# Performance work log

Hardware: AMD Instinct MI355X
Metric: run time of the kernel (lower is better)

## Reference

```python
import jax, jax.numpy as jnp
import numpy as np

B, S, D = 2, 1024, 1024
L, E, F = 2, 8, 2048


def setup_inputs() -> dict:
    key = jax.random.key(0)
    kx, kp, k1, k2 = jax.random.split(key, 4)
    x = jax.random.normal(kx, (B, S, D), dtype=jnp.float32)
    # prototypes scaled so dot products are O(1), keeping softmax well-behaved
    protos = jax.random.normal(kp, (L, E, D), dtype=jnp.float32) / np.sqrt(D)
    W1 = jax.random.normal(k1, (L, E, D, F), dtype=jnp.float32) * 0.02
    W2 = jax.random.normal(k2, (L, E, F, D), dtype=jnp.float32) * 0.02
    return {"x": x, "protos": protos, "W1": W1, "W2": W2, "k": 2}


def _route(x, protos_l, k):
    # expert_mapping: abs(dot(prototype, input)) per expert, keep top-k, rest -> -inf, softmax
    scores = jnp.abs(jnp.einsum("bsd,ed->bse", x, protos_l))  # [B,S,E]
    topv, _ = jax.lax.top_k(scores, k)
    thresh = topv[..., -1:]  # k-th largest per token
    masked = jnp.where(scores >= thresh, scores, -jnp.inf)
    return jax.nn.softmax(masked, axis=-1)  # [B,S,E]


def reference(x, protos, W1, W2, k):
    n_layers = protos.shape[0]
    for l in range(n_layers):  # fixed small layer loop
        w = _route(x, protos[l], k)  # [B,S,E]
        h = jax.nn.relu(jnp.einsum("bsd,edf->bsef", x, W1[l]))  # [B,S,E,F]
        y = jnp.einsum("bsef,efd,bse->bsd", h, W2[l], w)  # weighted expert mix
        x = x + y
    return x
```

## Files before the change

### kernel.cpp

```cpp
#include <hip/hip_runtime.h>
#include <hip/hip_bf16.h>
#include <cstdint>

#define T_TOKENS 2048
#define DDIM 1024
#define FDIM 2048
#define NEXP 8
#define NLAYER 2
#define BMPAD 64
#define RMAX 4608
#define RALLOC 4736

#define ATILE_EL 2048
#define BTILE_EL 4096

typedef unsigned short u16;
typedef short bf16x8 __attribute__((ext_vector_type(8)));
typedef u16 u16x8 __attribute__((ext_vector_type(8)));
typedef u16 u16x4v __attribute__((ext_vector_type(4)));
typedef float f32x4 __attribute__((ext_vector_type(4)));

#define VMCNT(n) asm volatile("s_waitcnt vmcnt(" #n ")" ::: "memory")
#define SB() __builtin_amdgcn_sched_barrier(0)
#define BAR() __builtin_amdgcn_s_barrier()

__device__ __forceinline__ u16 bf16_rn(float f) {
  unsigned u = __builtin_bit_cast(unsigned, f);
  u += 0x7fffu + ((u >> 16) & 1u);
  return (u16)(u >> 16);
}
__device__ __forceinline__ float bf16_f(u16 h) {
  unsigned u = ((unsigned)h) << 16;
  return __builtin_bit_cast(float, u);
}

__device__ __forceinline__ void gl16(const void* g, void* l) {
  __builtin_amdgcn_global_load_lds((const __attribute__((address_space(1))) void*)g,
                                   (__attribute__((address_space(3))) void*)l, 16, 0, 0);
}

__device__ __forceinline__ void xcd_swizzle(int& bx, int& by, int& bz) {
  const unsigned gx = gridDim.x, gy = gridDim.y;
  const unsigned lin = blockIdx.x + gx * (blockIdx.y + gy * blockIdx.z);
  const unsigned nwg = gx * gy * gridDim.z;
  const unsigned nl = (lin & 7u) * (nwg >> 3) + (lin >> 3);
  bx = nl % gx;
  const unsigned t = nl / gx;
  by = t % gy;
  bz = t / gy;
}

__global__ __launch_bounds__(256) void route_kernel(
    const float* __restrict__ x, const float* __restrict__ protos,
    int* __restrict__ eid, float* __restrict__ wgt) {
  const int t = blockIdx.x;
  const int tid = threadIdx.x;
  const float4* xr4 = (const float4*)(x + (size_t)t * DDIM);
  const float4* pr4 = (const float4*)protos;
  __shared__ float red[NEXP][256];
  const float4 xv = xr4[tid];
  float acc[NEXP];
#pragma unroll
  for (int e = 0; e < NEXP; ++e) {
    const float4 p = pr4[e * 256 + tid];
    acc[e] = xv.x * p.x + xv.y * p.y + xv.z * p.z + xv.w * p.w;
  }
#pragma unroll
  for (int e = 0; e < NEXP; ++e) red[e][tid] = acc[e];
  __syncthreads();
  for (int s = 128; s > 0; s >>= 1) {
    if (tid < s) {
#pragma unroll
      for (int e = 0; e < NEXP; ++e) red[e][tid] += red[e][tid + s];
    }
    __syncthreads();
  }
  if (tid == 0) {
    float m1 = -1.f, m2 = -1.f;
    int i1 = 0, i2 = 0;
#pragma unroll
    for (int e = 0; e < NEXP; ++e) {
      float s = fabsf(red[e][0]);
      if (s > m1) { m2 = m1; i2 = i1; m1 = s; i1 = e; }
      else if (s > m2) { m2 = s; i2 = e; }
    }
    float e2 = __expf(m2 - m1);
    float z = 1.f + e2;
    eid[t * 2] = i1;
    eid[t * 2 + 1] = i2;
    wgt[t * 2] = 1.f / z;
    wgt[t * 2 + 1] = e2 / z;
  }
}

__global__ __launch_bounds__(256) void route2_kernel(
    const float* __restrict__ x, const float* __restrict__ protos2,
    const u16* __restrict__ h_hi, const u16* __restrict__ h_lo,
    const float* __restrict__ P, const int* __restrict__ eidA,
    const int* __restrict__ pos, const float* __restrict__ wgtA,
    int* __restrict__ eidB, float* __restrict__ wgtB) {
  const int t = blockIdx.x;
  const int tid = threadIdx.x;
  __shared__ float red[NEXP][256];
  const float4 xv = ((const float4*)(x + (size_t)t * DDIM))[tid];
  float acc[NEXP];
#pragma unroll
  for (int e = 0; e < NEXP; ++e) {
    const float4 p = ((const float4*)protos2)[e * 256 + tid];
    acc[e] = xv.x * p.x + xv.y * p.y + xv.z * p.z + xv.w * p.w;
  }
  const int p0 = pos[t * 2], p1 = pos[t * 2 + 1];
  const int e0 = eidA[t * 2], e1 = eidA[t * 2 + 1];
  const float w0 = wgtA[t * 2], w1 = wgtA[t * 2 + 1];
  const int f0 = tid * 8;
  const int nkbF = FDIM >> 5;
  float h0[8], h1[8];
  {
    const size_t el0 = ((size_t)(p0 >> 6) * nkbF + (f0 >> 5)) * ATILE_EL +
                       (size_t)((((f0 >> 3) & 3) * 64 + (p0 & 63)) * 8);
    const size_t el1 = ((size_t)(p1 >> 6) * nkbF + (f0 >> 5)) * ATILE_EL +
                       (size_t)((((f0 >> 3) & 3) * 64 + (p1 & 63)) * 8);
    u16x8 a = *(const u16x8*)&h_hi[el0], b = *(const u16x8*)&h_lo[el0];
    u16x8 c = *(const u16x8*)&h_hi[el1], d = *(const u16x8*)&h_lo[el1];
#pragma unroll
    for (int j = 0; j < 8; ++j) {
      h0[j] = bf16_f(a[j]) + bf16_f(b[j]);
      h1[j] = bf16_f(c[j]) + bf16_f(d[j]);
    }
  }
#pragma unroll
  for (int e2 = 0; e2 < NEXP; ++e2) {
    const float* P0 = P + ((size_t)(e0 * NEXP + e2)) * FDIM + f0;
    const float* P1 = P + ((size_t)(e1 * NEXP + e2)) * FDIM + f0;
    float c = 0.f;
#pragma unroll
    for (int j = 0; j < 8; ++j) c += w0 * h0[j] * P0[j] + w1 * h1[j] * P1[j];
    acc[e2] += c;
  }
#pragma unroll
  for (int e = 0; e < NEXP; ++e) red[e][tid] = acc[e];
  __syncthreads();
  for (int s = 128; s > 0; s >>= 1) {
    if (tid < s) {
#pragma unroll
      for (int e = 0; e < NEXP; ++e) red[e][tid] += red[e][tid + s];
    }
    __syncthreads();
  }
  if (tid == 0) {
    float m1 = -1.f, m2 = -1.f;
    int i1 = 0, i2 = 0;
#pragma unroll
    for (int e = 0; e < NEXP; ++e) {
      float s = fabsf(red[e][0]);
      if (s > m1) { m2 = m1; i2 = i1; m1 = s; i1 = e; }
      else if (s > m2) { m2 = s; i2 = e; }
    }
    float e2 = __expf(m2 - m1);
    float z = 1.f + e2;
    eidB[t * 2] = i1;
    eidB[t * 2 + 1] = i2;
    wgtB[t * 2] = 1.f / z;
    wgtB[t * 2 + 1] = e2 / z;
  }
}

__global__ __launch_bounds__(256) void compact_kernel(
    const int* __restrict__ eid, int* __restrict__ cnt, int* __restrict__ offp,
    int* __restrict__ row2token, int* __restrict__ pos) {
  __shared__ int lcnt[NEXP][256];
  __shared__ int s_off[NEXP], s_tot[NEXP];
  const int tid = threadIdx.x;
  const int base = tid * 16;

  int my[16];
#pragma unroll
  for (int i = 0; i < 4; ++i)
    *(int4*)&my[i * 4] = *(const int4*)(eid + base + i * 4);

#pragma unroll
  for (int e = 0; e < NEXP; ++e) {
    int c = 0;
#pragma unroll
    for (int i = 0; i < 16; ++i) c += (my[i] == e) ? 1 : 0;
    lcnt[e][tid] = c;
  }

  for (int r = tid; r < RMAX; r += 256) row2token[r] = -1;
  __syncthreads();

  if (tid < NEXP) {
    int run = 0;
    for (int i = 0; i < 256; ++i) {
      int v = lcnt[tid][i];
      lcnt[tid][i] = run;
      run += v;
    }
    s_tot[tid] = run;
  }
  __syncthreads();
  if (tid == 0) {
    int o = 0;
    for (int e = 0; e < NEXP; ++e) {
      s_off[e] = o;
      o += (s_tot[e] + BMPAD - 1) & ~(BMPAD - 1);
    }
  }
  __syncthreads();

  int myoff[NEXP];
#pragma unroll
  for (int e = 0; e < NEXP; ++e) myoff[e] = s_off[e] + lcnt[e][tid];
#pragma unroll
  for (int i = 0; i < 16; ++i) {
    int r = 0;
#pragma unroll
    for (int e = 0; e < NEXP; ++e) r = (my[i] == e) ? myoff[e] : r;
    row2token[r] = (base + i) >> 1;
    pos[base + i] = r;
#pragma unroll
    for (int e = 0; e < NEXP; ++e) myoff[e] += (my[i] == e) ? 1 : 0;
  }

  if (tid < NEXP) {
    cnt[tid] = s_tot[tid];
    offp[tid] = s_off[tid];
  }
}

template <bool LO>
__global__ __launch_bounds__(256) void gather_kernel(
    const float* __restrict__ x, const int* __restrict__ row2token,
    u16* __restrict__ Ahi, u16* __restrict__ Alo) {
  const int r = blockIdx.x;
  const int t = row2token[r];
  const int c = threadIdx.x * 4;
  float4 v = make_float4(0.f, 0.f, 0.f, 0.f);
  if (t >= 0) v = *(const float4*)(x + (size_t)t * DDIM + c);
  float vv[4] = {v.x, v.y, v.z, v.w};
  u16x4v hi, lo;
#pragma unroll
  for (int i = 0; i < 4; ++i) {
    u16 h = bf16_rn(vv[i]);
    hi[i] = h;
    if (LO) lo[i] = bf16_rn(vv[i] - bf16_f(h));
  }
  const size_t el = ((size_t)(r >> 6) * (DDIM >> 5) + (c >> 5)) * ATILE_EL +
                    (size_t)(((c >> 3) & 3) * 64 + (r & 63)) * 8 + (c & 7);
  *(u16x4v*)(Ahi + el) = hi;
  if (LO) *(u16x4v*)(Alo + el) = lo;
}

template <bool LO>
__global__ __launch_bounds__(256) void wconv_kernel(
    const float* __restrict__ W, u16* __restrict__ Hi, u16* __restrict__ Lo,
    int K, int N) {
  const int e = blockIdx.z, nb = blockIdx.x, kb = blockIdx.y;
  const float* Wp = W + ((size_t)e * K + (size_t)kb * 32) * N + nb * 128;
  __shared__ float tile[32][129];
  const int t = threadIdx.x;
#pragma unroll
  for (int i = 0; i < 4; ++i) {
    const int f4 = i * 256 + t;
    const int kr = f4 >> 5;
    const int c4 = (f4 & 31) * 4;
    float4 v = *(const float4*)(Wp + (size_t)kr * N + c4);
    *(float4*)&tile[kr][c4] = v;
  }
  __syncthreads();
  const size_t tb = (((size_t)e * (N >> 7) + nb) * (K >> 5) + kb) * BTILE_EL;
#pragma unroll
  for (int j = 0; j < 2; ++j) {
    const int cid = j * 256 + t;
    const int n = cid & 127, ksel = cid >> 7;
    u16x8 hv, lv;
#pragma unroll
    for (int i = 0; i < 8; ++i) {
      float f = tile[ksel * 8 + i][n];
      u16 h = bf16_rn(f);
      hv[i] = h;
      if (LO) lv[i] = bf16_rn(f - bf16_f(h));
    }
    *(u16x8*)(Hi + tb + (size_t)cid * 8) = hv;
    if (LO) *(u16x8*)(Lo + tb + (size_t)cid * 8) = lv;
  }
}

__global__ __launch_bounds__(256) void wconv_p_kernel(
    const float* __restrict__ W, u16* __restrict__ Hi,
    const float* __restrict__ proto2, float* __restrict__ Ppart, int K, int N) {
  const int e = blockIdx.z, nb = blockIdx.x, kb = blockIdx.y;
  const float* Wp = W + ((size_t)e * K + (size_t)kb * 32) * N + nb * 128;
  __shared__ float tile[32][129];
  __shared__ float pr[NEXP][128];
  const int t = threadIdx.x;
#pragma unroll
  for (int i = 0; i < 4; ++i) {
    const int f4 = i * 256 + t;
    const int kr = f4 >> 5;
    const int c4 = (f4 & 31) * 4;
    float4 v = *(const float4*)(Wp + (size_t)kr * N + c4);
    *(float4*)&tile[kr][c4] = v;
  }
  {
    const int idx = t * 4;
    const int e2 = idx >> 7, n = idx & 127;
    *(float4*)&pr[e2][n] = *(const float4*)(proto2 + (size_t)e2 * DDIM + nb * 128 + n);
  }
  __syncthreads();
  const size_t tb = (((size_t)e * (N >> 7) + nb) * (K >> 5) + kb) * BTILE_EL;
#pragma unroll
  for (int j = 0; j < 2; ++j) {
    const int cid = j * 256 + t;
    const int n = cid & 127, ksel = cid >> 7;
    u16x8 hv;
#pragma unroll
    for (int i = 0; i < 8; ++i) hv[i] = bf16_rn(tile[ksel * 8 + i][n]);
    *(u16x8*)(Hi + tb + (size_t)cid * 8) = hv;
  }
  const int e2 = t >> 5, f = t & 31;
  float s = 0.f;
#pragma unroll 16
  for (int n = 0; n < 128; ++n) s += tile[f][n] * pr[e2][n];
  Ppart[(((size_t)nb * NEXP + e) * NEXP + e2) * FDIM + kb * 32 + f] = s;
}

__global__ __launch_bounds__(256) void reduce_p_kernel(
    const float* __restrict__ Ppart, float* __restrict__ P) {
  const int i = blockIdx.x * 256 + threadIdx.x;
  float s = 0.f;
#pragma unroll
  for (int nb = 0; nb < 8; ++nb) s += Ppart[(size_t)nb * (NEXP * NEXP * FDIM) + i];
  P[i] = s;
}

__global__ __launch_bounds__(256, 3) void gemm_split(
    const u16* __restrict__ Ahi, const u16* __restrict__ Alo,
    const u16* __restrict__ Bhi, const u16* __restrict__ Blo,
    u16* __restrict__ OutHi, u16* __restrict__ OutLo,
    const int* __restrict__ cnt, const int* __restrict__ offp, int K, int N) {
  int bx, by, bz;
  xcd_swizzle(bx, by, bz);
  const int e = bz;
  const int cp = (cnt[e] + 63) & ~63;
  if (by * 64 >= cp) return;
  const int row0 = offp[e] + by * 64;
  const int n0 = bx * 128;
  const int nkb = K >> 5;

  constexpr int BUF_EL = 12288;
  __shared__ u16 lds[2 * BUF_EL];

  const int tid = threadIdx.x;
  const int lane = tid & 63;
  const int wid = tid >> 6;
  const int wr = wid >> 1, wc = wid & 1;
  const int lr = lane & 15, kg = lane >> 4;
  const int lo16 = lane << 4;

  f32x4 acc[2][4];
#pragma unroll
  for (int i = 0; i < 2; ++i)
#pragma unroll
    for (int j = 0; j < 4; ++j)
#pragma unroll
      for (int r = 0; r < 4; ++r) acc[i][j][r] = 0.f;

  const size_t abase = (size_t)(row0 >> 6) * nkb;
  const size_t bbase = ((size_t)e * (N >> 7) + (n0 >> 7)) * nkb;

  auto STAGE = [&](int kb, int b) {
    char* d = (char*)(lds + b * BUF_EL);
    const char* gah = (const char*)(Ahi + (abase + kb) * ATILE_EL);
    const char* gal = (const char*)(Alo + (abase + kb) * ATILE_EL);
    const char* gbh = (const char*)(Bhi + (bbase + kb) * BTILE_EL);
    const char* gbl = (const char*)(Blo + (bbase + kb) * BTILE_EL);
    if (wid == 0) {
      gl16(gah + 0 * 1024 + lo16, d + 0 * 1024);
      gl16(gah + 1 * 1024 + lo16, d + 1 * 1024);
      gl16(gah + 2 * 1024 + lo16, d + 2 * 1024);
      gl16(gah + 3 * 1024 + lo16, d + 3 * 1024);
      gl16(gal + 0 * 1024 + lo16, d + 4096 + 0 * 1024);
      gl16(gal + 1 * 1024 + lo16, d + 4096 + 1 * 1024);
    } else if (wid == 1) {
// ... 51 lines not shown
#pragma unroll
    for (int j = 0; j < 4; ++j) {
      bf16x8 bl = *(const bf16x8*)&BsL[bcol + j * 128];
      acc[0][j] = __builtin_amdgcn_mfma_f32_16x16x32_bf16(ah0, bl, acc[0][j], 0, 0, 0);
      acc[1][j] = __builtin_amdgcn_mfma_f32_16x16x32_bf16(ah1, bl, acc[1][j], 0, 0, 0);
      acc[0][j] = __builtin_amdgcn_mfma_f32_16x16x32_bf16(al0, bh[j], acc[0][j], 0, 0, 0);
      acc[1][j] = __builtin_amdgcn_mfma_f32_16x16x32_bf16(al1, bh[j], acc[1][j], 0, 0, 0);
    }
    SB(); BAR(); SB();
    cur ^= 1;
  }

  const int nkbO = N >> 5;
#pragma unroll
  for (int i = 0; i < 2; ++i) {
#pragma unroll
    for (int j = 0; j < 4; ++j) {
      const int Cj = n0 + wc * 64 + j * 16 + lr;
      f32x4 v = acc[i][j];
#pragma unroll
      for (int r = 0; r < 4; ++r) {
        const int R = row0 + wr * 32 + i * 16 + kg * 4 + r;
        float f = fmaxf(v[r], 0.f);
        const size_t el = ((size_t)(R >> 6) * nkbO + (Cj >> 5)) * ATILE_EL +
                          (size_t)(((Cj >> 3) & 3) * 64 + (R & 63)) * 8 + (Cj & 7);
        u16 h = bf16_rn(f);
        OutHi[el] = h;
        OutLo[el] = bf16_rn(f - bf16_f(h));
      }
    }
  }
}

template <bool RELU, int OUTMODE, int SKF>
__global__ __launch_bounds__(256, 4) void gemm_plain(
    const u16* __restrict__ Ahi, const u16* __restrict__ Bhi,
    u16* __restrict__ OutHi, float* __restrict__ OutF,
    const int* __restrict__ cnt, const int* __restrict__ offp, int K, int N) {
  int bx, by, bz;
  xcd_swizzle(bx, by, bz);
  const int e = bz / SKF, sk = bz % SKF;
  const int cp = (cnt[e] + 63) & ~63;
  if (by * 128 >= cp) return;
  const int row0 = offp[e] + by * 128;
  const int rend = offp[e] + cp;
  const int n0 = bx * 128;
  const int nkb = K >> 5;
  const int kbN = nkb / SKF;
  const int kb0 = sk * kbN;

  constexpr int BUF_EL = 8192;
  __shared__ u16 lds[2 * BUF_EL];

  const int tid = threadIdx.x;
  const int lane = tid & 63;
  const int wid = tid >> 6;
  const int wr = wid >> 1, wc = wid & 1;
  const int lr = lane & 15, kg = lane >> 4;
  const int lo16 = lane << 4;

  f32x4 acc[4][4];
#pragma unroll
  for (int i = 0; i < 4; ++i)
#pragma unroll
    for (int j = 0; j < 4; ++j)
#pragma unroll
      for (int r = 0; r < 4; ++r) acc[i][j][r] = 0.f;

  const int at0 = row0 >> 6;
  const size_t bbase = ((size_t)e * (N >> 7) + (n0 >> 7)) * nkb;

  auto STAGE = [&](int kb, int b) {
    char* d = (char*)(lds + b * BUF_EL);
    if (wid < 2) {
      const char* g = (const char*)(Ahi + ((size_t)(at0 + wid) * nkb + kb) * ATILE_EL);
      gl16(g + 0 * 1024 + lo16, d + wid * 4096 + 0 * 1024);
      gl16(g + 1 * 1024 + lo16, d + wid * 4096 + 1 * 1024);
      gl16(g + 2 * 1024 + lo16, d + wid * 4096 + 2 * 1024);
      gl16(g + 3 * 1024 + lo16, d + wid * 4096 + 3 * 1024);
    } else {
      const char* g = (const char*)(Bhi + (bbase + kb) * BTILE_EL) + (wid - 2) * 4096;
      gl16(g + 0 * 1024 + lo16, d + 8192 + (wid - 2) * 4096 + 0 * 1024);
      gl16(g + 1 * 1024 + lo16, d + 8192 + (wid - 2) * 4096 + 1 * 1024);
      gl16(g + 2 * 1024 + lo16, d + 8192 + (wid - 2) * 4096 + 2 * 1024);
      gl16(g + 3 * 1024 + lo16, d + 8192 + (wid - 2) * 4096 + 3 * 1024);
    }
  };

  STAGE(kb0, 0);
  int cur = 0;
  for (int kb = kb0; kb < kb0 + kbN; ++kb) {
    const bool pf = (kb + 1 < kb0 + kbN);
    if (pf) STAGE(kb + 1, cur ^ 1);
    if (pf) { VMCNT(4); } else { VMCNT(0); }
    SB(); BAR(); SB();

    const u16* buf = lds + cur * BUF_EL;
    const u16* AsH = buf + wr * 2048;
    const u16* BsH = buf + 4096;
    const int arow = (kg * 64 + lr) * 8;
    const int bcol = (kg * 128 + wc * 64 + lr) * 8;

    bf16x8 ah[4], bh[4];
#pragma unroll
    for (int i = 0; i < 4; ++i) ah[i] = *(const bf16x8*)&AsH[arow + i * 128];
#pragma unroll
    for (int j = 0; j < 4; ++j) bh[j] = *(const bf16x8*)&BsH[bcol + j * 128];
#pragma unroll
    for (int i = 0; i < 4; ++i)
#pragma unroll
      for (int j = 0; j < 4; ++j)
        acc[i][j] = __builtin_amdgcn_mfma_f32_16x16x32_bf16(ah[i], bh[j], acc[i][j], 0, 0, 0);
    SB(); BAR(); SB();
    cur ^= 1;
  }

  const int nkbO = N >> 5;
#pragma unroll
  for (int i = 0; i < 4; ++i) {
#pragma unroll
    for (int j = 0; j < 4; ++j) {
      const int Cj = n0 + wc * 64 + j * 16 + lr;
      f32x4 v = acc[i][j];
#pragma unroll
      for (int r = 0; r < 4; ++r) {
        const int R = row0 + wr * 64 + i * 16 + kg * 4 + r;
        if (R >= rend) continue;
        float f = v[r];
        if (RELU) f = fmaxf(f, 0.f);
        if constexpr (OUTMODE == 0) {
          OutF[((size_t)sk * RALLOC + R) * N + Cj] = f;
        } else {
          const size_t el = ((size_t)(R >> 6) * nkbO + (Cj >> 5)) * ATILE_EL +
                            (size_t)(((Cj >> 3) & 3) * 64 + (R & 63)) * 8 + (Cj & 7);
          OutHi[el] = bf16_rn(f);
        }
      }
    }
  }
}

__global__ __launch_bounds__(256) void apply_kernel(
    const float* __restrict__ part, const int* __restrict__ pos,
    const float* __restrict__ wgt, float* __restrict__ x) {
  const int t = blockIdx.x;
  const int c = threadIdx.x * 4;
  const int p0 = pos[t * 2], p1 = pos[t * 2 + 1];
  const float w0 = wgt[t * 2], w1 = wgt[t * 2 + 1];
  const float* P1p = part + (size_t)RALLOC * DDIM;
  float4 xa = *(float4*)(x + (size_t)t * DDIM + c);
  float4 y0 = *(const float4*)(part + (size_t)p0 * DDIM + c);
  float4 y1 = *(const float4*)(part + (size_t)p1 * DDIM + c);
  const float4 b0 = *(const float4*)(P1p + (size_t)p0 * DDIM + c);
  const float4 b1 = *(const float4*)(P1p + (size_t)p1 * DDIM + c);
  y0.x += b0.x; y0.y += b0.y; y0.z += b0.z; y0.w += b0.w;
  y1.x += b1.x; y1.y += b1.y; y1.z += b1.z; y1.w += b1.w;
  xa.x += w0 * y0.x + w1 * y1.x;
  xa.y += w0 * y0.y + w1 * y1.y;
  xa.z += w0 * y0.z + w1 * y1.z;
  xa.w += w0 * y0.w + w1 * y1.w;
  *(float4*)(x + (size_t)t * DDIM + c) = xa;
}

extern "C" void kernel_launch(void* const* d_in, const int* in_sizes, int n_in,
                              void* d_out, int out_size, void* d_ws, size_t ws_size,
                              hipStream_t stream) {
  const float* x = (const float*)d_in[0];
  const float* protos = (const float*)d_in[1];
  const float* W1 = (const float*)d_in[2];
  const float* W2 = (const float*)d_in[3];
  float* xcur = (float*)d_out;

  u16* W_hi = (u16*)d_ws;
  u16* W_lo = W_hi + (size_t)NEXP * DDIM * FDIM;
  u16* Ag_hi = W_lo + (size_t)NEXP * DDIM * FDIM;
  u16* Ag_lo = Ag_hi + (size_t)RALLOC * DDIM;
  u16* h_hi = Ag_lo + (size_t)RALLOC * DDIM;
  u16* h_lo = h_hi + (size_t)RALLOC * FDIM;
  float* part = (float*)(h_lo + (size_t)RALLOC * FDIM);
  float* Ppart = part + (size_t)2 * RALLOC * DDIM;
  float* P = Ppart + (size_t)8 * NEXP * NEXP * FDIM;
  float* wgtA = P + (size_t)NEXP * NEXP * FDIM;
  float* wgtB = wgtA + T_TOKENS * 2;
  int* eidA = (int*)(wgtB + T_TOKENS * 2);
  int* eidB = eidA + T_TOKENS * 2;
  int* posA = eidB + T_TOKENS * 2;
  int* posB = posA + T_TOKENS * 2;
  int* cnt = posB + T_TOKENS * 2;
  int* offp = cnt + NEXP;
  int* row2token = offp + NEXP;

  hipMemcpyAsync(xcur, x, (size_t)T_TOKENS * DDIM * sizeof(float),
                 hipMemcpyDeviceToDevice, stream);

  const float* protos2 = protos + (size_t)NEXP * DDIM;

  route_kernel<<<T_TOKENS, 256, 0, stream>>>(xcur, protos, eidA, wgtA);
  compact_kernel<<<1, 256, 0, stream>>>(eidA, cnt, offp, row2token, posA);
  gather_kernel<true><<<RMAX, 256, 0, stream>>>(xcur, row2token, Ag_hi, Ag_lo);
  wconv_kernel<true><<<dim3(FDIM / 128, DDIM / 32, NEXP), 256, 0, stream>>>(
      W1, W_hi, W_lo, DDIM, FDIM);
  gemm_split<<<dim3(FDIM / 128, RMAX / 64, NEXP), 256, 0, stream>>>(
      Ag_hi, Ag_lo, W_hi, W_lo, h_hi, h_lo, cnt, offp, DDIM, FDIM);
  wconv_p_kernel<<<dim3(DDIM / 128, FDIM / 32, NEXP), 256, 0, stream>>>(
      W2, W_hi, protos2, Ppart, FDIM, DDIM);
  reduce_p_kernel<<<NEXP * NEXP * FDIM / 256, 256, 0, stream>>>(Ppart, P);
  gemm_plain<false, 0, 2><<<dim3(DDIM / 128, RMAX / 128, NEXP * 2), 256, 0, stream>>>(
      h_hi, W_hi, nullptr, part, cnt, offp, FDIM, DDIM);
  route2_kernel<<<T_TOKENS, 256, 0, stream>>>(
      xcur, protos2, h_hi, h_lo, P, eidA, posA, wgtA, eidB, wgtB);
  apply_kernel<<<T_TOKENS, 256, 0, stream>>>(part, posA, wgtA, xcur);

  compact_kernel<<<1, 256, 0, stream>>>(eidB, cnt, offp, row2token, posB);
  gather_kernel<false><<<RMAX, 256, 0, stream>>>(xcur, row2token, Ag_hi, nullptr);
  wconv_kernel<false><<<dim3(FDIM / 128, DDIM / 32, NEXP), 256, 0, stream>>>(
      W1 + (size_t)NEXP * DDIM * FDIM, W_hi, nullptr, DDIM, FDIM);
  gemm_plain<true, 2, 1><<<dim3(FDIM / 128, RMAX / 128, NEXP), 256, 0, stream>>>(
      Ag_hi, W_hi, h_hi, nullptr, cnt, offp, DDIM, FDIM);
  wconv_kernel<false><<<dim3(DDIM / 128, FDIM / 32, NEXP), 256, 0, stream>>>(
      W2 + (size_t)NEXP * FDIM * DDIM, W_hi, nullptr, FDIM, DDIM);
  gemm_plain<false, 0, 2><<<dim3(DDIM / 128, RMAX / 128, NEXP * 2), 256, 0, stream>>>(
      h_hi, W_hi, nullptr, part, cnt, offp, FDIM, DDIM);
  apply_kernel<<<T_TOKENS, 256, 0, stream>>>(part, posB, wgtB, xcur);
}
```

Before: 357.2 us.

## Fuse independent stages into multi-role kernels and drop split-K in down GEMM

Independent launches are merged into combined kernels that pick a role from the block index. Weight conversion runs alongside gather, the layer-1 split GEMM alongside the W2 conversion and projection, and the layer-1 down GEMM alongside the layer-2 weight conversions and the P reduction. Apply and compact are also merged into one launch. Split-K is removed from the down GEMM so apply reads one partial buffer, and a separate W2A buffer lets layer-2 weight conversion overlap layer-1 work. The aims are fewer launches and tail bubbles and better CU fill; the costs are less parallelism in the down GEMM and heterogeneous blocks sharing LDS and occupancy limits.

```diff
diff --git a/kernel.cpp b/kernel.cpp
--- a/kernel.cpp
+++ b/kernel.cpp
@@ -6,7 +6,6 @@
 #define DDIM 1024
 #define FDIM 2048
 #define NEXP 8
-#define NLAYER 2
 #define BMPAD 64
 #define RMAX 4608
 #define RALLOC 4736
@@ -33,206 +32,99 @@
   unsigned u = ((unsigned)h) << 16;
   return __builtin_bit_cast(float, u);
 }
-
 __device__ __forceinline__ void gl16(const void* g, void* l) {
   __builtin_amdgcn_global_load_lds((const __attribute__((address_space(1))) void*)g,
                                    (__attribute__((address_space(3))) void*)l, 16, 0, 0);
 }
 
-__device__ __forceinline__ void xcd_swizzle(int& bx, int& by, int& bz) {
-  const unsigned gx = gridDim.x, gy = gridDim.y;
-  const unsigned lin = blockIdx.x + gx * (blockIdx.y + gy * blockIdx.z);
-  const unsigned nwg = gx * gy * gridDim.z;
+template <int GX, int GY, int GZ>
+__device__ __forceinline__ void swz3(unsigned lin, int& bx, int& by, int& bz) {
+  constexpr unsigned nwg = (unsigned)GX * GY * GZ;
   const unsigned nl = (lin & 7u) * (nwg >> 3) + (lin >> 3);
-  bx = nl % gx;
-  const unsigned t = nl / gx;
-  by = t % gy;
-  bz = t / gy;
-}
-
-__global__ __launch_bounds__(256) void route_kernel(
-    const float* __restrict__ x, const float* __restrict__ protos,
-    int* __restrict__ eid, float* __restrict__ wgt) {
-  const int t = blockIdx.x;
-  const int tid = threadIdx.x;
-  const float4* xr4 = (const float4*)(x + (size_t)t * DDIM);
-  const float4* pr4 = (const float4*)protos;
-  __shared__ float red[NEXP][256];
-  const float4 xv = xr4[tid];
-  float acc[NEXP];
-#pragma unroll
-  for (int e = 0; e < NEXP; ++e) {
-    const float4 p = pr4[e * 256 + tid];
-    acc[e] = xv.x * p.x + xv.y * p.y + xv.z * p.z + xv.w * p.w;
-  }
-#pragma unroll
-  for (int e = 0; e < NEXP; ++e) red[e][tid] = acc[e];
+  bx = nl % GX;
+  const unsigned t = nl / GX;
+  by = t % GY;
+  bz = t / GY;
+}
+
+
+template <bool LO>
+__device__ __forceinline__ void wconv_dev(
+    int nb, int kb, int e, const float* __restrict__ W, u16* __restrict__ Hi,
+    u16* __restrict__ Lo, int K, int N, float* tile ) {
+  const float* Wp = W + ((size_t)e * K + (size_t)kb * 32) * N + nb * 128;
+  const int t = threadIdx.x;
+#pragma unroll
+  for (int i = 0; i < 4; ++i) {
+    const int f4 = i * 256 + t;
+    const int kr = f4 >> 5;
+    const int c4 = (f4 & 31) * 4;
+    float4 v = *(const float4*)(Wp + (size_t)kr * N + c4);
+    *(float4*)&tile[kr * 129 + c4] = v;
+  }
   __syncthreads();
-  for (int s = 128; s > 0; s >>= 1) {
-    if (tid < s) {
-#pragma unroll
-      for (int e = 0; e < NEXP; ++e) red[e][tid] += red[e][tid + s];
-    }
-    __syncthreads();
-  }
-  if (tid == 0) {
-    float m1 = -1.f, m2 = -1.f;
-    int i1 = 0, i2 = 0;
-#pragma unroll
-    for (int e = 0; e < NEXP; ++e) {
-      float s = fabsf(red[e][0]);
-      if (s > m1) { m2 = m1; i2 = i1; m1 = s; i1 = e; }
-      else if (s > m2) { m2 = s; i2 = e; }
-    }
-    float e2 = __expf(m2 - m1);
-    float z = 1.f + e2;
-    eid[t * 2] = i1;
-    eid[t * 2 + 1] = i2;
-    wgt[t * 2] = 1.f / z;
-    wgt[t * 2 + 1] = e2 / z;
-  }
-}
-
-__global__ __launch_bounds__(256) void route2_kernel(
-    const float* __restrict__ x, const float* __restrict__ protos2,
-    const u16* __restrict__ h_hi, const u16* __restrict__ h_lo,
-    const float* __restrict__ P, const int* __restrict__ eidA,
-    const int* __restrict__ pos, const float* __restrict__ wgtA,
-    int* __restrict__ eidB, float* __restrict__ wgtB) {
-  const int t = blockIdx.x;
-  const int tid = threadIdx.x;
-  __shared__ float red[NEXP][256];
-  const float4 xv = ((const float4*)(x + (size_t)t * DDIM))[tid];
-  float acc[NEXP];
-#pragma unroll
-  for (int e = 0; e < NEXP; ++e) {
-    const float4 p = ((const float4*)protos2)[e * 256 + tid];
-    acc[e] = xv.x * p.x + xv.y * p.y + xv.z * p.z + xv.w * p.w;
-  }
-  const int p0 = pos[t * 2], p1 = pos[t * 2 + 1];
-  const int e0 = eidA[t * 2], e1 = eidA[t * 2 + 1];
-  const float w0 = wgtA[t * 2], w1 = wgtA[t * 2 + 1];
-  const int f0 = tid * 8;
-  const int nkbF = FDIM >> 5;
-  float h0[8], h1[8];
+  const size_t tb = (((size_t)e * (N >> 7) + nb) * (K >> 5) + kb) * BTILE_EL;
+#pragma unroll
+  for (int j = 0; j < 2; ++j) {
+    const int cid = j * 256 + t;
+    const int n = cid & 127, ksel = cid >> 7;
+    u16x8 hv, lv;
+#pragma unroll
+    for (int i = 0; i < 8; ++i) {
+      float f = tile[(ksel * 8 + i) * 129 + n];
+      u16 h = bf16_rn(f);
+      hv[i] = h;
+      if (LO) lv[i] = bf16_rn(f - bf16_f(h));
+    }
+    *(u16x8*)(Hi + tb + (size_t)cid * 8) = hv;
+    if (LO) *(u16x8*)(Lo + tb + (size_t)cid * 8) = lv;
+  }
+}
+
+__device__ __forceinline__ void wconv_p_dev(
+    int nb, int kb, int e, const float* __restrict__ W, u16* __restrict__ Hi,
+    const float* __restrict__ proto2, float* __restrict__ Ppart, int K, int N,
+    float* smem) {
+  float* tile = smem;
+  float* pr = smem + 32 * 129;
+  const float* Wp = W + ((size_t)e * K + (size_t)kb * 32) * N + nb * 128;
+  const int t = threadIdx.x;
+#pragma unroll
+  for (int i = 0; i < 4; ++i) {
+    const int f4 = i * 256 + t;
+    const int kr = f4 >> 5;
+    const int c4 = (f4 & 31) * 4;
+    float4 v = *(const float4*)(Wp + (size_t)kr * N + c4);
+    *(float4*)&tile[kr * 129 + c4] = v;
+  }
   {
-    const size_t el0 = ((size_t)(p0 >> 6) * nkbF + (f0 >> 5)) * ATILE_EL +
-                       (size_t)((((f0 >> 3) & 3) * 64 + (p0 & 63)) * 8);
-    const size_t el1 = ((size_t)(p1 >> 6) * nkbF + (f0 >> 5)) * ATILE_EL +
-                       (size_t)((((f0 >> 3) & 3) * 64 + (p1 & 63)) * 8);
-    u16x8 a = *(const u16x8*)&h_hi[el0], b = *(const u16x8*)&h_lo[el0];
-    u16x8 c = *(const u16x8*)&h_hi[el1], d = *(const u16x8*)&h_lo[el1];
-#pragma unroll
-    for (int j = 0; j < 8; ++j) {
-      h0[j] = bf16_f(a[j]) + bf16_f(b[j]);
-      h1[j] = bf16_f(c[j]) + bf16_f(d[j]);
-    }
-  }
-#pragma unroll
-  for (int e2 = 0; e2 < NEXP; ++e2) {
-    const float* P0 = P + ((size_t)(e0 * NEXP + e2)) * FDIM + f0;
-    const float* P1 = P + ((size_t)(e1 * NEXP + e2)) * FDIM + f0;
-    float c = 0.f;
-#pragma unroll
-    for (int j = 0; j < 8; ++j) c += w0 * h0[j] * P0[j] + w1 * h1[j] * P1[j];
-    acc[e2] += c;
-  }
-#pragma unroll
-  for (int e = 0; e < NEXP; ++e) red[e][tid] = acc[e];
+    const int idx = t * 4;
+    const int e2 = idx >> 7, n = idx & 127;
+    *(float4*)&pr[e2 * 128 + n] =
+        *(const float4*)(proto2 + (size_t)e2 * DDIM + nb * 128 + n);
+  }
   __syncthreads();
-  for (int s = 128; s > 0; s >>= 1) {
-    if (tid < s) {
-#pragma unroll
-      for (int e = 0; e < NEXP; ++e) red[e][tid] += red[e][tid + s];
-    }
-    __syncthreads();
-  }
-  if (tid == 0) {
-    float m1 = -1.f, m2 = -1.f;
-    int i1 = 0, i2 = 0;
-#pragma unroll
-    for (int e = 0; e < NEXP; ++e) {
-      float s = fabsf(red[e][0]);
-      if (s > m1) { m2 = m1; i2 = i1; m1 = s; i1 = e; }
-      else if (s > m2) { m2 = s; i2 = e; }
-    }
-    float e2 = __expf(m2 - m1);
-    float z = 1.f + e2;
-    eidB[t * 2] = i1;
-    eidB[t * 2 + 1] = i2;
-    wgtB[t * 2] = 1.f / z;
-    wgtB[t * 2 + 1] = e2 / z;
-  }
-}
-
-__global__ __launch_bounds__(256) void compact_kernel(
-    const int* __restrict__ eid, int* __restrict__ cnt, int* __restrict__ offp,
-    int* __restrict__ row2token, int* __restrict__ pos) {
-  __shared__ int lcnt[NEXP][256];
-  __shared__ int s_off[NEXP], s_tot[NEXP];
-  const int tid = threadIdx.x;
-  const int base = tid * 16;
-
-  int my[16];
-#pragma unroll
-  for (int i = 0; i < 4; ++i)
-    *(int4*)&my[i * 4] = *(const int4*)(eid + base + i * 4);
-
-#pragma unroll
-  for (int e = 0; e < NEXP; ++e) {
-    int c = 0;
-#pragma unroll
-    for (int i = 0; i < 16; ++i) c += (my[i] == e) ? 1 : 0;
-    lcnt[e][tid] = c;
-  }
-
-  for (int r = tid; r < RMAX; r += 256) row2token[r] = -1;
-  __syncthreads();
-
-  if (tid < NEXP) {
-    int run = 0;
-    for (int i = 0; i < 256; ++i) {
-      int v = lcnt[tid][i];
-      lcnt[tid][i] = run;
-      run += v;
-    }
-    s_tot[tid] = run;
-  }
-  __syncthreads();
-  if (tid == 0) {
-    int o = 0;
-    for (int e = 0; e < NEXP; ++e) {
-      s_off[e] = o;
-      o += (s_tot[e] + BMPAD - 1) & ~(BMPAD - 1);
-    }
-  }
-  __syncthreads();
-
-  int myoff[NEXP];
-#pragma unroll
-  for (int e = 0; e < NEXP; ++e) myoff[e] = s_off[e] + lcnt[e][tid];
-#pragma unroll
-  for (int i = 0; i < 16; ++i) {
-    int r = 0;
-#pragma unroll
-    for (int e = 0; e < NEXP; ++e) r = (my[i] == e) ? myoff[e] : r;
-    row2token[r] = (base + i) >> 1;
-    pos[base + i] = r;
-#pragma unroll
-    for (int e = 0; e < NEXP; ++e) myoff[e] += (my[i] == e) ? 1 : 0;
-  }
-
-  if (tid < NEXP) {
-    cnt[tid] = s_tot[tid];
-    offp[tid] = s_off[tid];
-  }
+  const size_t tb = (((size_t)e * (N >> 7) + nb) * (K >> 5) + kb) * BTILE_EL;
+#pragma unroll
+  for (int j = 0; j < 2; ++j) {
+    const int cid = j * 256 + t;
+    const int n = cid & 127, ksel = cid >> 7;
+    u16x8 hv;
+#pragma unroll
+    for (int i = 0; i < 8; ++i) hv[i] = bf16_rn(tile[(ksel * 8 + i) * 129 + n]);
+    *(u16x8*)(Hi + tb + (size_t)cid * 8) = hv;
+  }
+  const int e2 = t >> 5, f = t & 31;
+  float s = 0.f;
+#pragma unroll 16
+  for (int n = 0; n < 128; ++n) s += tile[f * 129 + n] * pr[e2 * 128 + n];
+  Ppart[(((size_t)nb * NEXP + e) * NEXP + e2) * FDIM + kb * 32 + f] = s;
 }
 
 template <bool LO>
-__global__ __launch_bounds__(256) void gather_kernel(
-    const float* __restrict__ x, const int* __restrict__ row2token,
+__device__ __forceinline__ void gather_dev(
+    int r, const float* __restrict__ x, const int* __restrict__ row2token,
     u16* __restrict__ Ahi, u16* __restrict__ Alo) {
-  const int r = blockIdx.x;
   const int t = row2token[r];
   const int c = threadIdx.x * 4;
   float4 v = make_float4(0.f, 0.f, 0.f, 0.f);
@@ -251,105 +143,20 @@
   if (LO) *(u16x4v*)(Alo + el) = lo;
 }
 
-template <bool LO>
-__global__ __launch_bounds__(256) void wconv_kernel(
-    const float* __restrict__ W, u16* __restrict__ Hi, u16* __restrict__ Lo,
-    int K, int N) {
-  const int e = blockIdx.z, nb = blockIdx.x, kb = blockIdx.y;
-  const float* Wp = W + ((size_t)e * K + (size_t)kb * 32) * N + nb * 128;
-  __shared__ float tile[32][129];
-  const int t = threadIdx.x;
-#pragma unroll
-  for (int i = 0; i < 4; ++i) {
-    const int f4 = i * 256 + t;
-    const int kr = f4 >> 5;
-    const int c4 = (f4 & 31) * 4;
-    float4 v = *(const float4*)(Wp + (size_t)kr * N + c4);
-    *(float4*)&tile[kr][c4] = v;
-  }
-  __syncthreads();
-  const size_t tb = (((size_t)e * (N >> 7) + nb) * (K >> 5) + kb) * BTILE_EL;
-#pragma unroll
-  for (int j = 0; j < 2; ++j) {
-    const int cid = j * 256 + t;
-    const int n = cid & 127, ksel = cid >> 7;
-    u16x8 hv, lv;
-#pragma unroll
-    for (int i = 0; i < 8; ++i) {
-      float f = tile[ksel * 8 + i][n];
-      u16 h = bf16_rn(f);
-      hv[i] = h;
-      if (LO) lv[i] = bf16_rn(f - bf16_f(h));
-    }
-    *(u16x8*)(Hi + tb + (size_t)cid * 8) = hv;
-    if (LO) *(u16x8*)(Lo + tb + (size_t)cid * 8) = lv;
-  }
-}
-
-__global__ __launch_bounds__(256) void wconv_p_kernel(
-    const float* __restrict__ W, u16* __restrict__ Hi,
-    const float* __restrict__ proto2, float* __restrict__ Ppart, int K, int N) {
-  const int e = blockIdx.z, nb = blockIdx.x, kb = blockIdx.y;
-  const float* Wp = W + ((size_t)e * K + (size_t)kb * 32) * N + nb * 128;
-  __shared__ float tile[32][129];
-  __shared__ float pr[NEXP][128];
-  const int t = threadIdx.x;
-#pragma unroll
-  for (int i = 0; i < 4; ++i) {
-    const int f4 = i * 256 + t;
-    const int kr = f4 >> 5;
-    const int c4 = (f4 & 31) * 4;
-    float4 v = *(const float4*)(Wp + (size_t)kr * N + c4);
-    *(float4*)&tile[kr][c4] = v;
-  }
-  {
-    const int idx = t * 4;
-    const int e2 = idx >> 7, n = idx & 127;
-    *(float4*)&pr[e2][n] = *(const float4*)(proto2 + (size_t)e2 * DDIM + nb * 128 + n);
-  }
-  __syncthreads();
-  const size_t tb = (((size_t)e * (N >> 7) + nb) * (K >> 5) + kb) * BTILE_EL;
-#pragma unroll
-  for (int j = 0; j < 2; ++j) {
-    const int cid = j * 256 + t;
-    const int n = cid & 127, ksel = cid >> 7;
-    u16x8 hv;
-#pragma unroll
-    for (int i = 0; i < 8; ++i) hv[i] = bf16_rn(tile[ksel * 8 + i][n]);
-    *(u16x8*)(Hi + tb + (size_t)cid * 8) = hv;
-  }
-  const int e2 = t >> 5, f = t & 31;
-  float s = 0.f;
-#pragma unroll 16
-  for (int n = 0; n < 128; ++n) s += tile[f][n] * pr[e2][n];
-  Ppart[(((size_t)nb * NEXP + e) * NEXP + e2) * FDIM + kb * 32 + f] = s;
-}
-
-__global__ __launch_bounds__(256) void reduce_p_kernel(
-    const float* __restrict__ Ppart, float* __restrict__ P) {
-  const int i = blockIdx.x * 256 + threadIdx.x;
-  float s = 0.f;
-#pragma unroll
-  for (int nb = 0; nb < 8; ++nb) s += Ppart[(size_t)nb * (NEXP * NEXP * FDIM) + i];
-  P[i] = s;
-}
-
-__global__ __launch_bounds__(256, 3) void gemm_split(
-    const u16* __restrict__ Ahi, const u16* __restrict__ Alo,
+__device__ __forceinline__ void gemm_split_dev(
+    unsigned lin, u16* lds, const u16* __restrict__ Ahi, const u16* __restrict__ Alo,
     const u16* __restrict__ Bhi, const u16* __restrict__ Blo,
     u16* __restrict__ OutHi, u16* __restrict__ OutLo,
     const int* __restrict__ cnt, const int* __restrict__ offp, int K, int N) {
   int bx, by, bz;
-  xcd_swizzle(bx, by, bz);
+  swz3<FDIM / 128, RMAX / 64, NEXP>(lin, bx, by, bz);
   const int e = bz;
   const int cp = (cnt[e] + 63) & ~63;
   if (by * 64 >= cp) return;
   const int row0 = offp[e] + by * 64;
   const int n0 = bx * 128;
   const int nkb = K >> 5;
-
   constexpr int BUF_EL = 12288;
-  __shared__ u16 lds[2 * BUF_EL];
 
   const int tid = threadIdx.x;
   const int lane = tid & 63;
@@ -467,25 +274,21 @@
   }
 }
 
-template <bool RELU, int OUTMODE, int SKF>
-__global__ __launch_bounds__(256, 4) void gemm_plain(
-    const u16* __restrict__ Ahi, const u16* __restrict__ Bhi,
+template <int GX, int GY, bool RELU, int OUTMODE>
+__device__ __forceinline__ void gemm_plain_dev(
+    unsigned lin, u16* lds, const u16* __restrict__ Ahi, const u16* __restrict__ Bhi,
     u16* __restrict__ OutHi, float* __restrict__ OutF,
     const int* __restrict__ cnt, const int* __restrict__ offp, int K, int N) {
   int bx, by, bz;
-  xcd_swizzle(bx, by, bz);
-  const int e = bz / SKF, sk = bz % SKF;
+  swz3<GX, GY, NEXP>(lin, bx, by, bz);
+  const int e = bz;
   const int cp = (cnt[e] + 63) & ~63;
   if (by * 128 >= cp) return;
   const int row0 = offp[e] + by * 128;
   const int rend = offp[e] + cp;
   const int n0 = bx * 128;
   const int nkb = K >> 5;
-  const int kbN = nkb / SKF;
-  const int kb0 = sk * kbN;
-
   constexpr int BUF_EL = 8192;
-  __shared__ u16 lds[2 * BUF_EL];
 
   const int tid = threadIdx.x;
   const int lane = tid & 63;
@@ -522,10 +325,10 @@
     }
   };
 
-  STAGE(kb0, 0);
+  STAGE(0, 0);
   int cur = 0;
-  for (int kb = kb0; kb < kb0 + kbN; ++kb) {
-    const bool pf = (kb + 1 < kb0 + kbN);
+  for (int kb = 0; kb < nkb; ++kb) {
+    const bool pf = (kb + 1 < nkb);
     if (pf) STAGE(kb + 1, cur ^ 1);
     if (pf) { VMCNT(4); } else { VMCNT(0); }
     SB(); BAR(); SB();
@@ -564,7 +367,7 @@
         float f = v[r];
         if (RELU) f = fmaxf(f, 0.f);
         if constexpr (OUTMODE == 0) {
-          OutF[((size_t)sk * RALLOC + R) * N + Cj] = f;
+          OutF[(size_t)R * N + Cj] = f;
         } else {
           const size_t el = ((size_t)(R >> 6) * nkbO + (Cj >> 5)) * ATILE_EL +
                             (size_t)(((Cj >> 3) & 3) * 64 + (R & 63)) * 8 + (Cj & 7);
@@ -573,6 +376,290 @@
       }
     }
   }
+}
+
+
+__global__ __launch_bounds__(256) void route_kernel(
+    const float* __restrict__ x, const float* __restrict__ protos,
+    int* __restrict__ eid, float* __restrict__ wgt) {
+  const int t = blockIdx.x;
+  const int tid = threadIdx.x;
+  __shared__ float red[NEXP][256];
+  const float4 xv = ((const float4*)(x + (size_t)t * DDIM))[tid];
+  float acc[NEXP];
+#pragma unroll
+  for (int e = 0; e < NEXP; ++e) {
+    const float4 p = ((const float4*)protos)[e * 256 + tid];
+    acc[e] = xv.x * p.x + xv.y * p.y + xv.z * p.z + xv.w * p.w;
+  }
+#pragma unroll
+  for (int e = 0; e < NEXP; ++e) red[e][tid] = acc[e];
+  __syncthreads();
+  for (int s = 128; s > 0; s >>= 1) {
+    if (tid < s) {
+#pragma unroll
+      for (int e = 0; e < NEXP; ++e) red[e][tid] += red[e][tid + s];
+    }
+    __syncthreads();
+  }
+  if (tid == 0) {
+    float m1 = -1.f, m2 = -1.f;
+    int i1 = 0, i2 = 0;
+#pragma unroll
+    for (int e = 0; e < NEXP; ++e) {
+      float s = fabsf(red[e][0]);
+      if (s > m1) { m2 = m1; i2 = i1; m1 = s; i1 = e; }
+      else if (s > m2) { m2 = s; i2 = e; }
+    }
+    float e2 = __expf(m2 - m1);
+    float z = 1.f + e2;
+    eid[t * 2] = i1;
+    eid[t * 2 + 1] = i2;
+    wgt[t * 2] = 1.f / z;
+    wgt[t * 2 + 1] = e2 / z;
+  }
+}
+
+__global__ __launch_bounds__(256) void route2_kernel(
+    const float* __restrict__ x, const float* __restrict__ protos2,
+    const u16* __restrict__ h_hi, const u16* __restrict__ h_lo,
+    const float* __restrict__ P, const int* __restrict__ eidA,
+    const int* __restrict__ pos, const float* __restrict__ wgtA,
+    int* __restrict__ eidB, float* __restrict__ wgtB) {
+  const int t = blockIdx.x;
+  const int tid = threadIdx.x;
+  __shared__ float red[NEXP][256];
+  const float4 xv = ((const float4*)(x + (size_t)t * DDIM))[tid];
+  float acc[NEXP];
+#pragma unroll
+  for (int e = 0; e < NEXP; ++e) {
+    const float4 p = ((const float4*)protos2)[e * 256 + tid];
+    acc[e] = xv.x * p.x + xv.y * p.y + xv.z * p.z + xv.w * p.w;
+  }
+  const int p0 = pos[t * 2], p1 = pos[t * 2 + 1];
+  const int e0 = eidA[t * 2], e1 = eidA[t * 2 + 1];
+  const float w0 = wgtA[t * 2], w1 = wgtA[t * 2 + 1];
+  const int f0 = tid * 8;
+  const int nkbF = FDIM >> 5;
+  float h0[8], h1[8];
+  {
+    const size_t el0 = ((size_t)(p0 >> 6) * nkbF + (f0 >> 5)) * ATILE_EL +
+                       (size_t)((((f0 >> 3) & 3) * 64 + (p0 & 63)) * 8);
+    const size_t el1 = ((size_t)(p1 >> 6) * nkbF + (f0 >> 5)) * ATILE_EL +
+                       (size_t)((((f0 >> 3) & 3) * 64 + (p1 & 63)) * 8);
+    u16x8 a = *(const u16x8*)&h_hi[el0], b = *(const u16x8*)&h_lo[el0];
+    u16x8 c = *(const u16x8*)&h_hi[el1], d = *(const u16x8*)&h_lo[el1];
+#pragma unroll
+    for (int j = 0; j < 8; ++j) {
+      h0[j] = bf16_f(a[j]) + bf16_f(b[j]);
+      h1[j] = bf16_f(c[j]) + bf16_f(d[j]);
+    }
+  }
+#pragma unroll
+  for (int e2 = 0; e2 < NEXP; ++e2) {
+    const float* P0 = P + ((size_t)(e0 * NEXP + e2)) * FDIM + f0;
+    const float* P1 = P + ((size_t)(e1 * NEXP + e2)) * FDIM + f0;
+    float c = 0.f;
+#pragma unroll
+    for (int j = 0; j < 8; ++j) c += w0 * h0[j] * P0[j] + w1 * h1[j] * P1[j];
+    acc[e2] += c;
+  }
+#pragma unroll
+  for (int e = 0; e < NEXP; ++e) red[e][tid] = acc[e];
+  __syncthreads();
+  for (int s = 128; s > 0; s >>= 1) {
+    if (tid < s) {
+#pragma unroll
+      for (int e = 0; e < NEXP; ++e) red[e][tid] += red[e][tid + s];
+    }
+    __syncthreads();
+  }
+  if (tid == 0) {
+    float m1 = -1.f, m2 = -1.f;
+    int i1 = 0, i2 = 0;
+#pragma unroll
+    for (int e = 0; e < NEXP; ++e) {
+      float s = fabsf(red[e][0]);
+      if (s > m1) { m2 = m1; i2 = i1; m1 = s; i1 = e; }
+      else if (s > m2) { m2 = s; i2 = e; }
+    }
+    float e2 = __expf(m2 - m1);
+    float z = 1.f + e2;
+    eidB[t * 2] = i1;
+    eidB[t * 2 + 1] = i2;
+    wgtB[t * 2] = 1.f / z;
+    wgtB[t * 2 + 1] = e2 / z;
+  }
+}
+
+__device__ __forceinline__ void compact_dev(
+    const int* __restrict__ eid, int* __restrict__ cnt, int* __restrict__ offp,
+    int* __restrict__ row2token, int* __restrict__ pos, int* lcnt ) {
+  int* s_off = lcnt + NEXP * 256;
+  int* s_tot = s_off + NEXP;
+  const int tid = threadIdx.x;
+  const int base = tid * 16;
+  int my[16];
+#pragma unroll
+  for (int i = 0; i < 4; ++i)
+    *(int4*)&my[i * 4] = *(const int4*)(eid + base + i * 4);
+#pragma unroll
+  for (int e = 0; e < NEXP; ++e) {
+    int c = 0;
+#pragma unroll
+    for (int i = 0; i < 16; ++i) c += (my[i] == e) ? 1 : 0;
+    lcnt[e * 256 + tid] = c;
+  }
+  for (int r = tid; r < RMAX; r += 256) row2token[r] = -1;
+  __syncthreads();
+  if (tid < NEXP) {
+    int run = 0;
+    for (int i = 0; i < 256; ++i) {
+      int v = lcnt[tid * 256 + i];
+      lcnt[tid * 256 + i] = run;
+      run += v;
+    }
+    s_tot[tid] = run;
+  }
+  __syncthreads();
+  if (tid == 0) {
+    int o = 0;
+    for (int e = 0; e < NEXP; ++e) {
+      s_off[e] = o;
+      o += (s_tot[e] + BMPAD - 1) & ~(BMPAD - 1);
+    }
+  }
+  __syncthreads();
+  int myoff[NEXP];
+#pragma unroll
+  for (int e = 0; e < NEXP; ++e) myoff[e] = s_off[e] + lcnt[e * 256 + tid];
+#pragma unroll
+  for (int i = 0; i < 16; ++i) {
+    int r = 0;
+#pragma unroll
+    for (int e = 0; e < NEXP; ++e) r = (my[i] == e) ? myoff[e] : r;
+    row2token[r] = (base + i) >> 1;
+    pos[base + i] = r;
+#pragma unroll
+    for (int e = 0; e < NEXP; ++e) myoff[e] += (my[i] == e) ? 1 : 0;
+  }
+  if (tid < NEXP) {
+    cnt[tid] = s_tot[tid];
+    offp[tid] = s_off[tid];
+  }
+}
+
+__global__ __launch_bounds__(256) void compact_kernel(
+    const int* __restrict__ eid, int* __restrict__ cnt, int* __restrict__ offp,
+    int* __restrict__ row2token, int* __restrict__ pos) {
+  __shared__ int lcnt[NEXP * 256 + 16];
+  compact_dev(eid, cnt, offp, row2token, pos, lcnt);
+}
+
+__global__ __launch_bounds__(256) void fusedC1_kernel(
+    const float* __restrict__ W1, u16* __restrict__ W_hi, u16* __restrict__ W_lo,
+    const float* __restrict__ x, const int* __restrict__ row2token,
+    u16* __restrict__ Ag_hi, u16* __restrict__ Ag_lo) {
+  __shared__ float smem[32 * 129];
+  const unsigned lin = blockIdx.x;
+  if (lin < 4096u) {
+    const int nb = lin % 16;
+    const int kb = (lin / 16) % 32;
+    const int e = lin / 512;
+    wconv_dev<true>(nb, kb, e, W1, W_hi, W_lo, DDIM, FDIM, smem);
+  } else {
+    gather_dev<true>((int)(lin - 4096u), x, row2token, Ag_hi, Ag_lo);
+  }
+}
+
+__global__ __launch_bounds__(256, 3) void fusedC2_kernel(
+    const u16* __restrict__ Ag_hi, const u16* __restrict__ Ag_lo,
+    const u16* __restrict__ W_hi, const u16* __restrict__ W_lo,
+    u16* __restrict__ h_hi, u16* __restrict__ h_lo,
+    const int* __restrict__ cnt, const int* __restrict__ offp,
+    const float* __restrict__ W2, u16* __restrict__ W2A,
+    const float* __restrict__ proto2, float* __restrict__ Ppart) {
+  __shared__ u16 lds[2 * 12288];
+  const unsigned lin = blockIdx.x;
+  if (lin < 9216u) {
+    gemm_split_dev(lin, lds, Ag_hi, Ag_lo, W_hi, W_lo, h_hi, h_lo, cnt, offp,
+                   DDIM, FDIM);
+  } else {
+    const unsigned l2 = lin - 9216u;
+    const int nb = l2 % 8;
+    const int kb = (l2 / 8) % 64;
+    const int e = l2 / 512;
+    wconv_p_dev(nb, kb, e, W2, W2A, proto2, Ppart, FDIM, DDIM, (float*)lds);
+  }
+}
+
+__global__ __launch_bounds__(256, 4) void fusedC3_kernel(
+    const u16* __restrict__ h_hi, const u16* __restrict__ W2A,
+    float* __restrict__ part, const int* __restrict__ cnt, const int* __restrict__ offp,
+    const float* __restrict__ W1b, u16* __restrict__ W_lo,
+    const float* __restrict__ W2b, u16* __restrict__ W_hi,
+    const float* __restrict__ Ppart, float* __restrict__ P) {
+  __shared__ u16 lds[2 * 8192];
+  const unsigned lin = blockIdx.x;
+  if (lin < 2304u) {
+    gemm_plain_dev<DDIM / 128, RMAX / 128, false, 0>(
+        lin, lds, h_hi, W2A, nullptr, part, cnt, offp, FDIM, DDIM);
+  } else if (lin < 6400u) {
+    const unsigned l2 = lin - 2304u;
+    wconv_dev<false>(l2 % 16, (l2 / 16) % 32, l2 / 512, W1b, W_lo, nullptr,
+                     DDIM, FDIM, (float*)lds);
+  } else if (lin < 10496u) {
+    const unsigned l2 = lin - 6400u;
+    wconv_dev<false>(l2 % 8, (l2 / 8) % 64, l2 / 512, W2b, W_hi, nullptr,
+                     FDIM, DDIM, (float*)lds);
+  } else {
+    const int i = (int)(lin - 10496u) * 256 + threadIdx.x;
+    float s = 0.f;
+#pragma unroll
+    for (int nb = 0; nb < 8; ++nb) s += Ppart[(size_t)nb * (NEXP * NEXP * FDIM) + i];
+    P[i] = s;
+  }
+}
+
+__global__ __launch_bounds__(256) void fusedD_kernel(
+    const float* __restrict__ part, const int* __restrict__ pos,
+    const float* __restrict__ wgt, float* __restrict__ x,
+    const int* __restrict__ eidB, int* __restrict__ cnt, int* __restrict__ offp,
+    int* __restrict__ row2token, int* __restrict__ posB) {
+  __shared__ int lcnt[NEXP * 256 + 16];
+  const unsigned lin = blockIdx.x;
+  if (lin < 2048u) {
+    const int t = lin;
+    const int c = threadIdx.x * 4;
+    const int p0 = pos[t * 2], p1 = pos[t * 2 + 1];
+    const float w0 = wgt[t * 2], w1 = wgt[t * 2 + 1];
+    float4 xa = *(float4*)(x + (size_t)t * DDIM + c);
+    const float4 y0 = *(const float4*)(part + (size_t)p0 * DDIM + c);
+    const float4 y1 = *(const float4*)(part + (size_t)p1 * DDIM + c);
+    xa.x += w0 * y0.x + w1 * y1.x;
+    xa.y += w0 * y0.y + w1 * y1.y;
+    xa.z += w0 * y0.z + w1 * y1.z;
+    xa.w += w0 * y0.w + w1 * y1.w;
+    *(float4*)(x + (size_t)t * DDIM + c) = xa;
+  } else {
+    compact_dev(eidB, cnt, offp, row2token, posB, lcnt);
+  }
+}
+
+__global__ __launch_bounds__(256) void gather_kernel(
+    const float* __restrict__ x, const int* __restrict__ row2token,
+    u16* __restrict__ Ahi) {
+  gather_dev<false>(blockIdx.x, x, row2token, Ahi, nullptr);
+}
+
+template <int GX, bool RELU, int OUTMODE>
+__global__ __launch_bounds__(256, 4) void gemm_plain_kernel(
+    const u16* __restrict__ Ahi, const u16* __restrict__ Bhi,
+    u16* __restrict__ OutHi, float* __restrict__ OutF,
+    const int* __restrict__ cnt, const int* __restrict__ offp, int K, int N) {
+  __shared__ u16 lds[2 * 8192];
+  gemm_plain_dev<GX, RMAX / 128, RELU, OUTMODE>(blockIdx.x, lds, Ahi, Bhi, OutHi,
+                                                OutF, cnt, offp, K, N);
 }
 
 __global__ __launch_bounds__(256) void apply_kernel(
@@ -582,14 +669,9 @@
   const int c = threadIdx.x * 4;
   const int p0 = pos[t * 2], p1 = pos[t * 2 + 1];
   const float w0 = wgt[t * 2], w1 = wgt[t * 2 + 1];
-  const float* P1p = part + (size_t)RALLOC * DDIM;
   float4 xa = *(float4*)(x + (size_t)t * DDIM + c);
-  float4 y0 = *(const float4*)(part + (size_t)p0 * DDIM + c);
-  float4 y1 = *(const float4*)(part + (size_t)p1 * DDIM + c);
-  const float4 b0 = *(const float4*)(P1p + (size_t)p0 * DDIM + c);
-  const float4 b1 = *(const float4*)(P1p + (size_t)p1 * DDIM + c);
-  y0.x += b0.x; y0.y += b0.y; y0.z += b0.z; y0.w += b0.w;
-  y1.x += b1.x; y1.y += b1.y; y1.z += b1.z; y1.w += b1.w;
+  const float4 y0 = *(const float4*)(part + (size_t)p0 * DDIM + c);
+  const float4 y1 = *(const float4*)(part + (size_t)p1 * DDIM + c);
   xa.x += w0 * y0.x + w1 * y1.x;
   xa.y += w0 * y0.y + w1 * y1.y;
   xa.z += w0 * y0.z + w1 * y1.z;
@@ -608,12 +690,13 @@
 
   u16* W_hi = (u16*)d_ws;
   u16* W_lo = W_hi + (size_t)NEXP * DDIM * FDIM;
-  u16* Ag_hi = W_lo + (size_t)NEXP * DDIM * FDIM;
+  u16* W2A = W_lo + (size_t)NEXP * DDIM * FDIM;
+  u16* Ag_hi = W2A + (size_t)NEXP * DDIM * FDIM;
   u16* Ag_lo = Ag_hi + (size_t)RALLOC * DDIM;
   u16* h_hi = Ag_lo + (size_t)RALLOC * DDIM;
   u16* h_lo = h_hi + (size_t)RALLOC * FDIM;
   float* part = (float*)(h_lo + (size_t)RALLOC * FDIM);
-  float* Ppart = part + (size_t)2 * RALLOC * DDIM;
+  float* Ppart = part + (size_t)RALLOC * DDIM;
   float* P = Ppart + (size_t)8 * NEXP * NEXP * FDIM;
   float* wgtA = P + (size_t)NEXP * NEXP * FDIM;
   float* wgtB = wgtA + T_TOKENS * 2;
@@ -629,32 +712,26 @@
                  hipMemcpyDeviceToDevice, stream);
 
   const float* protos2 = protos + (size_t)NEXP * DDIM;
+  const float* W1b = W1 + (size_t)NEXP * DDIM * FDIM;
+  const float* W2b = W2 + (size_t)NEXP * FDIM * DDIM;
 
   route_kernel<<<T_TOKENS, 256, 0, stream>>>(xcur, protos, eidA, wgtA);
   compact_kernel<<<1, 256, 0, stream>>>(eidA, cnt, offp, row2token, posA);
-  gather_kernel<true><<<RMAX, 256, 0, stream>>>(xcur, row2token, Ag_hi, Ag_lo);
-  wconv_kernel<true><<<dim3(FDIM / 128, DDIM / 32, NEXP), 256, 0, stream>>>(
-      W1, W_hi, W_lo, DDIM, FDIM);
-  gemm_split<<<dim3(FDIM / 128, RMAX / 64, NEXP), 256, 0, stream>>>(
-      Ag_hi, Ag_lo, W_hi, W_lo, h_hi, h_lo, cnt, offp, DDIM, FDIM);
-  wconv_p_kernel<<<dim3(DDIM / 128, FDIM / 32, NEXP), 256, 0, stream>>>(
-      W2, W_hi, protos2, Ppart, FDIM, DDIM);
-  reduce_p_kernel<<<NEXP * NEXP * FDIM / 256, 256, 0, stream>>>(Ppart, P);
-  gemm_plain<false, 0, 2><<<dim3(DDIM / 128, RMAX / 128, NEXP * 2), 256, 0, stream>>>(
-      h_hi, W_hi, nullptr, part, cnt, offp, FDIM, DDIM);
+  fusedC1_kernel<<<4096 + RMAX, 256, 0, stream>>>(
+      W1, W_hi, W_lo, xcur, row2token, Ag_hi, Ag_lo);
+  fusedC2_kernel<<<9216 + 4096, 256, 0, stream>>>(
+      Ag_hi, Ag_lo, W_hi, W_lo, h_hi, h_lo, cnt, offp, W2, W2A, protos2, Ppart);
+  fusedC3_kernel<<<2304 + 4096 + 4096 + 512, 256, 0, stream>>>(
+      h_hi, W2A, part, cnt, offp, W1b, W_lo, W2b, W_hi, Ppart, P);
   route2_kernel<<<T_TOKENS, 256, 0, stream>>>(
       xcur, protos2, h_hi, h_lo, P, eidA, posA, wgtA, eidB, wgtB);
-  apply_kernel<<<T_TOKENS, 256, 0, stream>>>(part, posA, wgtA, xcur);
-
-  compact_kernel<<<1, 256, 0, stream>>>(eidB, cnt, offp, row2token, posB);
-  gather_kernel<false><<<RMAX, 256, 0, stream>>>(xcur, row2token, Ag_hi, nullptr);
-  wconv_kernel<false><<<dim3(FDIM / 128, DDIM / 32, NEXP), 256, 0, stream>>>(
-      W1 + (size_t)NEXP * DDIM * FDIM, W_hi, nullptr, DDIM, FDIM);
-  gemm_plain<true, 2, 1><<<dim3(FDIM / 128, RMAX / 128, NEXP), 256, 0, stream>>>(
-      Ag_hi, W_hi, h_hi, nullptr, cnt, offp, DDIM, FDIM);
-  wconv_kernel<false><<<dim3(DDIM / 128, FDIM / 32, NEXP), 256, 0, stream>>>(
-      W2 + (size_t)NEXP * FDIM * DDIM, W_hi, nullptr, FDIM, DDIM);
-  gemm_plain<false, 0, 2><<<dim3(DDIM / 128, RMAX / 128, NEXP * 2), 256, 0, stream>>>(
+  fusedD_kernel<<<2048 + 1, 256, 0, stream>>>(
+      part, posA, wgtA, xcur, eidB, cnt, offp, row2token, posB);
+
+  gather_kernel<<<RMAX, 256, 0, stream>>>(xcur, row2token, Ag_hi);
+  gemm_plain_kernel<FDIM / 128, true, 2><<<(FDIM / 128) * (RMAX / 128) * NEXP, 256, 0, stream>>>(
+      Ag_hi, W_lo, h_hi, nullptr, cnt, offp, DDIM, FDIM);
+  gemm_plain_kernel<DDIM / 128, false, 0><<<(DDIM / 128) * (RMAX / 128) * NEXP, 256, 0, stream>>>(
       h_hi, W_hi, nullptr, part, cnt, offp, FDIM, DDIM);
   apply_kernel<<<T_TOKENS, 256, 0, stream>>>(part, posB, wgtB, xcur);
 }
```

Measured after the change: 331.3 us. 7.2% less time.
